# Optimization experiments

Measured on AMD Instinct MI355X. Metric: run time of the kernel, lower is better.

## Reference

```python
import jax, jax.numpy as jnp
import numpy as np

B, L, H, V = 16, 1024, 512, 32000
HALF = H // 2
ALPHA = 0.95
EPS_NORM = 1e-12
EPS_LN = 1e-5


def setup_inputs() -> dict:
    key = jax.random.key(0)
    ks = jax.random.split(key, 12)
    s = 0.02
    return {
        "seq": jax.random.randint(ks[0], (B, L), 0, V),
        "embed": jax.random.normal(ks[1], (V, H), jnp.float32) * s,
        "ff_w1": jax.random.normal(ks[2], (2 * H, H), jnp.float32) * s,
        "ff_b1": jnp.zeros((2 * H,), jnp.float32),
        "ff_w2": jax.random.normal(ks[3], (H, 2 * H), jnp.float32) * s,
        "ff_b2": jnp.zeros((H,), jnp.float32),
        "gamma": jnp.ones((H,), jnp.float32),
        "beta": jnp.zeros((H,), jnp.float32),
        "sem_w": jax.random.normal(ks[4], (HALF, H), jnp.float32) * s,
        "epi_w": jax.random.normal(ks[5], (HALF, H), jnp.float32) * s,
        "rp_w": jax.random.normal(ks[6], (H, H), jnp.float32) * s,
        "rp_b": jnp.zeros((H,), jnp.float32),
        "out_w": jax.random.normal(ks[7], (V, H), jnp.float32) * s,
        "out_b": jnp.zeros((V,), jnp.float32),
    }


def _layernorm(x, gamma, beta):
    mu = jnp.mean(x, axis=-1, keepdims=True)
    var = jnp.mean(jnp.square(x - mu), axis=-1, keepdims=True)
    return (x - mu) * jax.lax.rsqrt(var + EPS_LN) * gamma + beta


def _l2norm(k):
    # F.normalize: k / max(||k||_2, eps)
    n = jnp.sqrt(jnp.sum(jnp.square(k), axis=-1, keepdims=True))
    return k / jnp.maximum(n, EPS_NORM)


def reference(seq, embed, ff_w1, ff_b1, ff_w2, ff_b2, gamma, beta,
              sem_w, epi_w, rp_w, rp_b, out_w, out_b):
    h = embed[seq]  # [B, L, H]
    ff = jnp.maximum(jnp.einsum('blh,fh->blf', h, ff_w1) + ff_b1, 0.0)
    ff = jnp.einsum('blf,hf->blh', ff, ff_w2) + ff_b2
    h = _layernorm(h + ff, gamma, beta)  # [B, L, H]

    # precompute all keys, time-major for scan: [L, B, half]
    ks_all = jnp.einsum('blh,ch->lbc', h, sem_w)
    ke_all = jnp.einsum('blh,ch->lbc', h, epi_w)

    def step(carry, inp):
        Ms, Me = carry                      # [B, half, half]
        ks, ke = inp                        # [B, half]
        kns = _l2norm(ks)
        kne = _l2norm(ke)
        vps = jnp.einsum('bij,bj->bi', Ms, kns)
        vpe = jnp.einsum('bij,bj->bi', Me, kne)
        Ds = (ks - vps)[:, :, None] * kns[:, None, :]
        De = (ke - vpe)[:, :, None] * kne[:, None, :]
        Ms = Ms + (1.0 - ALPHA) * Ds
        Me = Me + (1.0 - ALPHA) * De
        return (Ms, Me), None

    M0 = jnp.zeros((B, HALF, HALF), h.dtype)
    (M_s, M_e), _ = jax.lax.scan(step, (M0, M0), (ks_all[:L - 1], ke_all[:L - 1]))

    qs = ks_all[L - 1]  # sem_p(h[:, -1])
    qe = ke_all[L - 1]  # epi_p(h[:, -1])
    cs = jnp.einsum('bij,bj->bi', M_s, qs)
    ce = jnp.einsum('bij,bj->bi', M_e, qe)
    c = jnp.concatenate([cs, ce], axis=-1)  # [B, H]
    r = jnp.einsum('bh,gh->bg', c, rp_w) + rp_b
    return jnp.einsum('bh,vh->bv', r, out_w) + out_b  # [B, V]
```

## Files before the change

### kernel.cpp

```cpp
#include <hip/hip_runtime.h>
#include <stdint.h>

#define Bsz 16
#define Lsz 1024
#define Hsz 512
#define Vsz 32000
#define HALF 256
#define BETA 0.05f

typedef unsigned short u16;
typedef __attribute__((ext_vector_type(8))) short short8;
typedef __attribute__((ext_vector_type(4))) float f32x4;

__device__ __forceinline__ float bf2f(u16 u) { return __uint_as_float(((unsigned int)u) << 16); }
__device__ __forceinline__ u16 f2bf(float f) {
    unsigned int u = __float_as_uint(f);
    return (u16)((u + 0x7FFFu + ((u >> 16) & 1u)) >> 16);
}
__device__ __forceinline__ bool mode_f32(const void* gamma) {
    return *(const unsigned int*)gamma == 0x3F800000u;
}

__device__ __forceinline__ float wave_sum(float p) {
    p += __shfl_xor(p, 32, 64);
    p += __shfl_xor(p, 16, 64);
    p += __shfl_xor(p, 8, 64);
    p += __shfl_xor(p, 4, 64);
    p += __shfl_xor(p, 2, 64);
    p += __shfl_xor(p, 1, 64);
    return p;
}

__device__ __forceinline__ void cvt8(const void* src, u16* dst, int i, bool f32m) {
    union { u16 u[8]; uint4 q; } o;
    if (f32m) {
        const float* s = (const float*)src + i;
        const float4 a = *(const float4*)s;
        const float4 b = *(const float4*)(s + 4);
        o.u[0] = f2bf(a.x); o.u[1] = f2bf(a.y); o.u[2] = f2bf(a.z); o.u[3] = f2bf(a.w);
        o.u[4] = f2bf(b.x); o.u[5] = f2bf(b.y); o.u[6] = f2bf(b.z); o.u[7] = f2bf(b.w);
    } else {
        o.q = *(const uint4*)((const u16*)src + i);
    }
    *(uint4*)(dst + i) = o.q;
}

__global__ __launch_bounds__(256)
void cvt_all(const void* s0, const void* s1, const void* s2, const void* s3,
             const void* s4, const void* s5, const void* s6, const void* s7,
             const void* s8, const void* s9, const void* s10,
             u16* d0, u16* d1, u16* d2, u16* d3, u16* d4, u16* d5, u16* d6,
             u16* d7, u16* d8, u16* d9, u16* d10, const void* gamma) {
    const bool f32m = mode_f32(gamma);
    const int g = blockIdx.x * 256 + threadIdx.x;
    const void* src; u16* dst; int off;
    if      (g < 65536)  { src = s0;  dst = d0;  off = g; }
    else if (g < 131072) { src = s1;  dst = d1;  off = g - 65536; }
    else if (g < 147456) { src = s2;  dst = d2;  off = g - 131072; }
    else if (g < 163840) { src = s3;  dst = d3;  off = g - 147456; }
    else if (g < 196608) { src = s4;  dst = d4;  off = g - 163840; }
    else if (g < 196736) { src = s5;  dst = d5;  off = g - 196608; }
    else if (g < 196800) { src = s6;  dst = d6;  off = g - 196736; }
    else if (g < 196864) { src = s7;  dst = d7;  off = g - 196800; }
    else if (g < 196928) { src = s8;  dst = d8;  off = g - 196864; }
    else if (g < 196992) { src = s9;  dst = d9;  off = g - 196928; }
    else if (g < 200992) { src = s10; dst = d10; off = g - 196992; }
    else return;
    cvt8(src, dst, off * 8, f32m);
}

__global__ __launch_bounds__(256)
void gather_kernel(const int* __restrict__ seq, const void* __restrict__ embed,
                   u16* __restrict__ h0, const void* __restrict__ gamma) {
    const bool f32m = mode_f32(gamma);
    const int row = blockIdx.x * 4 + (threadIdx.x >> 6);
    const int lane = threadIdx.x & 63;
    const int tok = seq[row];
    union { u16 u[8]; uint4 q; } o;
    if (f32m) {
        const float* e = (const float*)embed + (size_t)tok * Hsz + lane * 8;
        const float4 a = *(const float4*)e;
        const float4 b = *(const float4*)(e + 4);
        o.u[0] = f2bf(a.x); o.u[1] = f2bf(a.y); o.u[2] = f2bf(a.z); o.u[3] = f2bf(a.w);
        o.u[4] = f2bf(b.x); o.u[5] = f2bf(b.y); o.u[6] = f2bf(b.z); o.u[7] = f2bf(b.w);
    } else {
        o.q = *((const uint4*)((const u16*)embed + (size_t)tok * Hsz) + lane);
    }
    *((uint4*)(h0 + (size_t)row * Hsz) + lane) = o.q;
}

template <int EPI>
__global__ __launch_bounds__(256)
void gemm128(const u16* __restrict__ A, const u16* __restrict__ B0,
             const u16* __restrict__ B1, const u16* __restrict__ bias,
             const u16* resid, void* Cout, int M, int N, int K) {
    __shared__ u16 Als[128 * 32];
    __shared__ u16 Bls[128 * 32];
    const int tid = threadIdx.x;
    const int wave = tid >> 6, lane = tid & 63;
    const int m0 = blockIdx.y * 128, n0 = blockIdx.x * 128;

    const u16* Bt;
    if (EPI == 2) Bt = (n0 < HALF) ? (B0 + (size_t)n0 * K) : (B1 + (size_t)(n0 - HALF) * K);
    else          Bt = B0 + (size_t)n0 * K;
    const u16* At = A + (size_t)m0 * K;

    const int wm = wave >> 1, wn = wave & 1;
    const int srow = lane >> 2;
    const int sk = (lane & 3) * 8;
    const int fr = lane & 15;
    const int fq = (lane >> 4) * 8;

    f32x4 acc[4][4];
#pragma unroll
    for (int i = 0; i < 4; i++)
#pragma unroll
        for (int j = 0; j < 4; j++) acc[i][j] = (f32x4){0.f, 0.f, 0.f, 0.f};

    for (int k0 = 0; k0 < K; k0 += 32) {
        __syncthreads();
#pragma unroll
        for (int c = 0; c < 2; c++) {
            const int ch = wave * 2 + c;
            const int row = ch * 16 + srow;
            __builtin_amdgcn_global_load_lds(
                (const __attribute__((address_space(1))) uint32_t*)(At + (size_t)row * K + k0 + sk),
                (__attribute__((address_space(3))) uint32_t*)(&Als[ch * 512]), 16, 0, 0);
            __builtin_amdgcn_global_load_lds(
                (const __attribute__((address_space(1))) uint32_t*)(Bt + (size_t)row * K + k0 + sk),
                (__attribute__((address_space(3))) uint32_t*)(&Bls[ch * 512]), 16, 0, 0);
        }
        __syncthreads();
        short8 af[4], bfr[4];
#pragma unroll
        for (int i = 0; i < 4; i++)
            af[i] = *(const short8*)&Als[(wm * 64 + i * 16 + fr) * 32 + fq];
#pragma unroll
        for (int j = 0; j < 4; j++)
            bfr[j] = *(const short8*)&Bls[(wn * 64 + j * 16 + fr) * 32 + fq];
#pragma unroll
        for (int i = 0; i < 4; i++)
#pragma unroll
            for (int j = 0; j < 4; j++)
                acc[i][j] = __builtin_amdgcn_mfma_f32_16x16x32_bf16(af[i], bfr[j], acc[i][j], 0, 0, 0);
    }

#pragma unroll
    for (int i = 0; i < 4; i++) {
#pragma unroll
        for (int j = 0; j < 4; j++) {
            const int n = n0 + wn * 64 + j * 16 + fr;
#pragma unroll
            for (int r = 0; r < 4; r++) {
                const int m = m0 + wm * 64 + i * 16 + (lane >> 4) * 4 + r;
                float v = acc[i][j][r];
                if (EPI == 0) {
                    v += bf2f(bias[n]);
                    v = v > 0.f ? v : 0.f;
                    ((u16*)Cout)[(size_t)m * N + n] = f2bf(v);
                } else if (EPI == 1) {
                    v += bf2f(bias[n]) + bf2f(resid[(size_t)m * N + n]);
                    ((u16*)Cout)[(size_t)m * N + n] = f2bf(v);
                } else {
                    const int mem = n >> 8, col = n & 255;
                    const int b = m >> 10, t = m & 1023;
                    ((u16*)Cout)[((size_t)(mem * Bsz + b) * Lsz + t) * HALF + col] = f2bf(v);
                }
            }
        }
    }
}

__global__ __launch_bounds__(256)
void ln_kernel(const u16* hs, const u16* __restrict__ gamma,
               const u16* __restrict__ beta, u16* hn) {
    const int row = blockIdx.x * 4 + (threadIdx.x >> 6);
    const int lane = threadIdx.x & 63;
    const uint4 raw = *(const uint4*)(hs + (size_t)row * Hsz + lane * 8);
    const u16* xr = (const u16*)&raw;
    float v[8];
#pragma unroll
    for (int j = 0; j < 8; j++) v[j] = bf2f(xr[j]);
    float s = 0.f;
#pragma unroll
    for (int j = 0; j < 8; j++) s += v[j];
    s = wave_sum(s);
    const float mu = s * (1.f / 512.f);
    float q = 0.f;
#pragma unroll
    for (int j = 0; j < 8; j++) { v[j] -= mu; q += v[j] * v[j]; }
    q = wave_sum(q);
    const float rstd = rsqrtf(q * (1.f / 512.f) + 1e-5f);
    union { u16 u[8]; uint4 qv; } o;
#pragma unroll
    for (int j = 0; j < 8; j++) {
        const int n = lane * 8 + j;
        o.u[j] = f2bf(v[j] * rstd * bf2f(gamma[n]) + bf2f(beta[n]));
    }
    *(uint4*)(hn + (size_t)row * Hsz + lane * 8) = o.qv;
}

__global__ __launch_bounds__(256)
void normalize_kernel(u16* kb, float* __restrict__ norms) {
    const int row = blockIdx.x * 4 + (threadIdx.x >> 6);
    const int lane = threadIdx.x & 63;
    u16* p = kb + (size_t)row * HALF + lane * 4;
    uint2 raw = *(uint2*)p;
    const u16* kp = (const u16*)&raw;
    float f[4];
#pragma unroll
    for (int j = 0; j < 4; j++) f[j] = bf2f(kp[j]);
    float s = f[0]*f[0] + f[1]*f[1] + f[2]*f[2] + f[3]*f[3];
    s = wave_sum(s);
    const float n = fmaxf(sqrtf(s), 1e-12f);
    const float inv = 1.f / n;
    union { u16 u[4]; uint2 q; } o;
#pragma unroll
    for (int j = 0; j < 4; j++) o.u[j] = f2bf(f[j] * inv);
    *(uint2*)p = o.q;
    if (lane == 0) norms[row] = n;
}

__global__ __launch_bounds__(256)
void gram_kernel(const u16* __restrict__ kn, float* __restrict__ G) {
    __shared__ u16 ls[64 * 264];
    const int mb = blockIdx.x, c = blockIdx.y;
    const int tid = threadIdx.x;
    const u16* src = kn + ((size_t)mb * Lsz + c * 64) * HALF;
    {
        const int row = tid >> 2, p = tid & 3;
        const u16* sp = src + row * 256 + p * 64;
        u16* dp = ls + row * 264 + p * 64;
#pragma unroll
        for (int i = 0; i < 8; i++)
            *(uint4*)(dp + i * 8) = *(const uint4*)(sp + i * 8);
    }
    __syncthreads();
    const int wave = tid >> 6, lane = tid & 63;
    const int fr = lane & 15, fq = (lane >> 4) * 8;
    f32x4 acc[4];
#pragma unroll
    for (int j = 0; j < 4; j++) acc[j] = (f32x4){0.f, 0.f, 0.f, 0.f};
    for (int k0 = 0; k0 < 256; k0 += 32) {
        const short8 a = *(const short8*)&ls[(wave * 16 + fr) * 264 + k0 + fq];
#pragma unroll
        for (int j = 0; j < 4; j++) {
            const short8 b = *(const short8*)&ls[(j * 16 + fr) * 264 + k0 + fq];
            acc[j] = __builtin_amdgcn_mfma_f32_16x16x32_bf16(a, b, acc[j], 0, 0, 0);
        }
    }
    float* gout = G + ((size_t)mb * 16 + c) * 4096;
#pragma unroll
    for (int j = 0; j < 4; j++)
#pragma unroll
        for (int r = 0; r < 4; r++)
            gout[(wave * 16 + (lane >> 4) * 4 + r) * 64 + j * 16 + fr] = acc[j][r];
}

__global__ __launch_bounds__(256)
void scan2_kernel(const u16* __restrict__ kn, const float* __restrict__ norms,
                  const float* __restrict__ G, float* __restrict__ cbuf) {
    __shared__ float uL[256], dL[64], sL[64], s2L[64];
    const int mb = blockIdx.x;
    const int tid = threadIdx.x, wave = tid >> 6, lane = tid & 63;
    const u16* knb = kn + (size_t)mb * Lsz * HALF;
    const float* nb = norms + (size_t)mb * Lsz;

    float u = bf2f(knb[1023 * HALF + tid]) * nb[1023];
    float cacc = 0.f;
    uL[tid] = u;
    __syncthreads();

    for (int c = 15; c >= 0; --c) {
        {
            const int t = tid >> 2, p = tid & 3;
            const u16* krow = knb + (size_t)(c * 64 + t) * HALF + p * 64;
            float part = 0.f;
#pragma unroll
            for (int jj = 0; jj < 64; jj += 8) {
                const short8 kv = *(const short8*)(krow + jj);
                const u16* kp = (const u16*)&kv;
                const f32x4 u0 = *(const f32x4*)&uL[p * 64 + jj];
                const f32x4 u1 = *(const f32x4*)&uL[p * 64 + jj + 4];
                part += bf2f(kp[0]) * u0[0] + bf2f(kp[1]) * u0[1]
                      + bf2f(kp[2]) * u0[2] + bf2f(kp[3]) * u0[3]
                      + bf2f(kp[4]) * u1[0] + bf2f(kp[5]) * u1[1]
                      + bf2f(kp[6]) * u1[2] + bf2f(kp[7]) * u1[3];
            }
            part += __shfl_xor(part, 1, 64);
            part += __shfl_xor(part, 2, 64);
            if (p == 0) dL[t] = part;
        }
        __syncthreads();
        if (wave == 0) {
            const float* grow = G + ((size_t)mb * 16 + c) * 4096 + lane * 64;
            float g[64];
#pragma unroll
            for (int q = 0; q < 64; q += 4) {
                const f32x4 gv = *(const f32x4*)(grow + q);
                g[q] = gv[0]; g[q + 1] = gv[1]; g[q + 2] = gv[2]; g[q + 3] = gv[3];
            }
#pragma unroll
            for (int q = 0; q < 64; q++) g[q] = (q > lane) ? g[q] : 0.f;
            const float d = dL[lane];
            const float mynorm = nb[c * 64 + lane];
            float r = 0.f;
            const bool lastchunk = (c == 15);
#pragma unroll
            for (int tp = 63; tp >= 0; --tp) {
                float cand = d - BETA * r;
                if (lastchunk && tp == 63) cand = 0.f;
                const float s = __shfl(cand, tp, 64);
                if (lane == tp) { sL[tp] = s; s2L[tp] = s * mynorm; }
                r += g[tp] * s;
            }
        }
        __syncthreads();
        {
            const u16* kcol = knb + (size_t)c * 64 * HALF + tid;
            float du = 0.f, dc = 0.f;
#pragma unroll 8
            for (int t2 = 0; t2 < 64; t2++) {
                const float kv = bf2f(kcol[(size_t)t2 * HALF]);
                du += sL[t2] * kv;
                dc += s2L[t2] * kv;
            }
            u -= BETA * du;
            cacc += BETA * dc;
            uL[tid] = u;
        }
        __syncthreads();
    }
    const int b = mb & 15, mem = mb >> 4;
    cbuf[(size_t)b * Hsz + mem * HALF + tid] = cacc;
}

__global__ __launch_bounds__(256)
void rproj_kernel(const float* __restrict__ cbuf, const u16* __restrict__ rpw,
                  const u16* __restrict__ rpb, u16* __restrict__ rbuf) {
    __shared__ float cl[Hsz];
    const int b = blockIdx.x, tid = threadIdx.x;
    cl[tid] = cbuf[(size_t)b * Hsz + tid];
    cl[tid + 256] = cbuf[(size_t)b * Hsz + 256 + tid];
    __syncthreads();
#pragma unroll
    for (int gg = 0; gg < 2; gg++) {
        const int g = gg * 256 + tid;
        const u16* wr = rpw + (size_t)g * Hsz;
        float acc = bf2f(rpb[g]);
        for (int k = 0; k < Hsz; k += 8) {
            const uint4 w8 = *(const uint4*)(wr + k);
            const u16* w = (const u16*)&w8;
            const float4 c0 = *(const float4*)&cl[k];
            const float4 c1 = *(const float4*)&cl[k + 4];
            acc += bf2f(w[0]) * c0.x + bf2f(w[1]) * c0.y + bf2f(w[2]) * c0.z + bf2f(w[3]) * c0.w
                 + bf2f(w[4]) * c1.x + bf2f(w[5]) * c1.y + bf2f(w[6]) * c1.z + bf2f(w[7]) * c1.w;
        }
        rbuf[(size_t)b * Hsz + g] = f2bf(acc);
    }
}

__global__ __launch_bounds__(256)
void logits_kernel(const u16* __restrict__ rbuf, const void* __restrict__ outw,
                   const u16* __restrict__ outb, void* __restrict__ out,
                   const void* __restrict__ gamma) {
    __shared__ u16 rls[16 * Hsz];
    const bool f32m = mode_f32(gamma);
    const int tid = threadIdx.x;
    {
        const uint4* src = (const uint4*)rbuf;
        uint4* dst = (uint4*)rls;
#pragma unroll
        for (int i = 0; i < 4; i++) dst[i * 256 + tid] = src[i * 256 + tid];
    }
    __syncthreads();
    const int wave = tid >> 6, lane = tid & 63;
    const int n0 = blockIdx.x * 256 + wave * 64;
    const int fr = lane & 15, fq = (lane >> 4) * 8;
    f32x4 acc[4];
#pragma unroll
    for (int j = 0; j < 4; j++) acc[j] = (f32x4){0.f, 0.f, 0.f, 0.f};
    if (f32m) {
        for (int k0 = 0; k0 < Hsz; k0 += 32) {
            const short8 af = *(const short8*)&rls[fr * Hsz + k0 + fq];
#pragma unroll
            for (int j = 0; j < 4; j++) {
                const float* wp = (const float*)outw + (size_t)(n0 + j * 16 + fr) * Hsz + k0 + fq;
                const float4 a = *(const float4*)wp;
                const float4 bq = *(const float4*)(wp + 4);
                union { u16 u[8]; short8 v; } bb;
                bb.u[0] = f2bf(a.x); bb.u[1] = f2bf(a.y); bb.u[2] = f2bf(a.z); bb.u[3] = f2bf(a.w);
                bb.u[4] = f2bf(bq.x); bb.u[5] = f2bf(bq.y); bb.u[6] = f2bf(bq.z); bb.u[7] = f2bf(bq.w);
                acc[j] = __builtin_amdgcn_mfma_f32_16x16x32_bf16(af, bb.v, acc[j], 0, 0, 0);
            }
        }
    } else {
        for (int k0 = 0; k0 < Hsz; k0 += 32) {
            const short8 af = *(const short8*)&rls[fr * Hsz + k0 + fq];
#pragma unroll
            for (int j = 0; j < 4; j++) {
                const short8 b8 = *(const short8*)((const u16*)outw + (size_t)(n0 + j * 16 + fr) * Hsz + k0 + fq);
                acc[j] = __builtin_amdgcn_mfma_f32_16x16x32_bf16(af, b8, acc[j], 0, 0, 0);
            }
        }
    }
#pragma unroll
    for (int j = 0; j < 4; j++) {
        const int v = n0 + j * 16 + fr;
        const float bv = bf2f(outb[v]);
#pragma unroll
        for (int r = 0; r < 4; r++) {
            const int bb = (lane >> 4) * 4 + r;
            const float val = acc[j][r] + bv;
            if (f32m) ((float*)out)[(size_t)bb * Vsz + v] = val;
            else      ((u16*)out)[(size_t)bb * Vsz + v] = f2bf(val);
        }
    }
}

extern "C" void kernel_launch(void* const* d_in, const int* in_sizes, int n_in,
                              void* d_out, int out_size, void* d_ws, size_t ws_size,
                              hipStream_t stream) {
    const int*  seq   = (const int*)d_in[0];
    const void* embed = d_in[1];
    const void* ffw1  = d_in[2];
    const void* ffb1  = d_in[3];
    const void* ffw2  = d_in[4];
    const void* ffb2  = d_in[5];
    const void* gamma = d_in[6];
    const void* beta  = d_in[7];
    const void* semw  = d_in[8];
    const void* epiw  = d_in[9];
    const void* rpw   = d_in[10];
    const void* rpb   = d_in[11];
    const void* outw  = d_in[12];
    const void* outb  = d_in[13];

    char* ws = (char*)d_ws;
    u16*   h0    = (u16*)(ws + 0);
    u16*   C1    = (u16*)(ws + (size_t)0x1000000);
    u16*   kbuf  = (u16*)(ws + (size_t)0x1000000);
    float* Gbuf  = (float*)(ws + (size_t)0x2000000);
    float* norms = (float*)(ws + (size_t)0x2800000);
    size_t off   = 50331648;
    u16* cffw1 = (u16*)(ws + off); off += (size_t)1024 * 512 * 2;
    u16* cffw2 = (u16*)(ws + off); off += (size_t)512 * 1024 * 2;
    u16* csemw = (u16*)(ws + off); off += (size_t)256 * 512 * 2;
    u16* cepiw = (u16*)(ws + off); off += (size_t)256 * 512 * 2;
    u16* crpw  = (u16*)(ws + off); off += (size_t)512 * 512 * 2;
    u16* cffb1 = (u16*)(ws + off); off += 1024 * 2;
    u16* cffb2 = (u16*)(ws + off); off += 512 * 2;
    u16* cgam  = (u16*)(ws + off); off += 512 * 2;
    u16* cbet  = (u16*)(ws + off); off += 512 * 2;
    u16* crpb  = (u16*)(ws + off); off += 512 * 2;
    u16* coutb = (u16*)(ws + off); off += (size_t)32000 * 2;
    off = (off + 255) & ~(size_t)255;
    float* cbuf = (float*)(ws + off); off += (size_t)16 * 512 * 4;
    u16*   rbuf = (u16*)(ws + off);

    cvt_all<<<786, 256, 0, stream>>>(ffw1, ffw2, semw, epiw, rpw, ffb1, ffb2,
                                     gamma, beta, rpb, outb,
                                     cffw1, cffw2, csemw, cepiw, crpw, cffb1, cffb2,
                                     cgam, cbet, crpb, coutb, gamma);
    gather_kernel<<<4096, 256, 0, stream>>>(seq, embed, h0, gamma);
    gemm128<0><<<dim3(8, 128), 256, 0, stream>>>(h0, cffw1, nullptr, cffb1, nullptr, C1,
                                                 16384, 1024, 512);
    gemm128<1><<<dim3(4, 128), 256, 0, stream>>>(C1, cffw2, nullptr, cffb2, h0, h0,
                                                 16384, 512, 1024);
    ln_kernel<<<4096, 256, 0, stream>>>(h0, cgam, cbet, h0);
    gemm128<2><<<dim3(4, 128), 256, 0, stream>>>(h0, csemw, cepiw, nullptr, nullptr, kbuf,
                                                 16384, 512, 512);
    normalize_kernel<<<8192, 256, 0, stream>>>(kbuf, norms);
    gram_kernel<<<dim3(32, 16), 256, 0, stream>>>(kbuf, Gbuf);
    scan2_kernel<<<32, 256, 0, stream>>>(kbuf, norms, Gbuf, cbuf);
    rproj_kernel<<<16, 256, 0, stream>>>(cbuf, crpw, crpb, rbuf);
    logits_kernel<<<125, 256, 0, stream>>>(rbuf, outw, coutb, d_out, gamma);
}
```

Before: 442.5 us.

## Prefetch next key chunk and G block into LDS with register double-buffering in scan2

The backward scan kernel now stages each 64-row chunk of normalized keys and its Gram block into shared memory. The loads for the next chunk are issued into registers at the start of each iteration and written to LDS after the current chunk finishes. This hides global-memory latency behind the serial per-chunk work and replaces repeated strided global reads with LDS reads. In exchange it uses more LDS and more registers, and adds one extra barrier per chunk.

```diff
diff --git a/kernel.cpp b/kernel.cpp
--- a/kernel.cpp
+++ b/kernel.cpp
@@ -7,6 +7,8 @@
 #define Vsz 32000
 #define HALF 256
 #define BETA 0.05f
+#define LSTRIDE 264
+#define GSTRIDE 68
 
 typedef unsigned short u16;
 typedef __attribute__((ext_vector_type(8))) short short8;
@@ -260,26 +262,54 @@
 __global__ __launch_bounds__(256)
 void scan2_kernel(const u16* __restrict__ kn, const float* __restrict__ norms,
                   const float* __restrict__ G, float* __restrict__ cbuf) {
+    __shared__ u16 ls[64 * LSTRIDE];
+    __shared__ float GS[64 * GSTRIDE];
     __shared__ float uL[256], dL[64], sL[64], s2L[64];
     const int mb = blockIdx.x;
     const int tid = threadIdx.x, wave = tid >> 6, lane = tid & 63;
     const u16* knb = kn + (size_t)mb * Lsz * HALF;
     const float* nb = norms + (size_t)mb * Lsz;
+    const float* gb = G + (size_t)mb * 16 * 4096;
+
+    const int srow = tid >> 2, scol = (tid & 3) * 64;
+    const int gcol = (tid & 3) * 16;
 
     float u = bf2f(knb[1023 * HALF + tid]) * nb[1023];
+    uL[tid] = u;
     float cacc = 0.f;
-    uL[tid] = u;
+
+    {
+        const uint4* s4 = (const uint4*)(knb + (size_t)15 * 64 * HALF + srow * HALF + scol);
+        u16* dp = ls + srow * LSTRIDE + scol;
+#pragma unroll
+        for (int i = 0; i < 8; i++) *(uint4*)(dp + i * 8) = s4[i];
+        const float4* g4 = (const float4*)(gb + (size_t)15 * 4096 + srow * 64 + gcol);
+        float* gp = GS + srow * GSTRIDE + gcol;
+#pragma unroll
+        for (int i = 0; i < 4; i++) *(float4*)(gp + i * 4) = g4[i];
+    }
     __syncthreads();
 
     for (int c = 15; c >= 0; --c) {
+        uint4 kv[8]; float4 gv[4];
+        if (c > 0) {
+            const uint4* s4 = (const uint4*)(knb + (size_t)(c - 1) * 64 * HALF + srow * HALF + scol);
+#pragma unroll
+            for (int i = 0; i < 8; i++) kv[i] = s4[i];
+            const float4* g4 = (const float4*)(gb + (size_t)(c - 1) * 4096 + srow * 64 + gcol);
+#pragma unroll
+            for (int i = 0; i < 4; i++) gv[i] = g4[i];
+        }
+        const float mynorm = (wave == 0) ? nb[c * 64 + lane] : 0.f;
+
         {
             const int t = tid >> 2, p = tid & 3;
-            const u16* krow = knb + (size_t)(c * 64 + t) * HALF + p * 64;
+            const u16* krow = ls + t * LSTRIDE + p * 64;
             float part = 0.f;
 #pragma unroll
             for (int jj = 0; jj < 64; jj += 8) {
-                const short8 kv = *(const short8*)(krow + jj);
-                const u16* kp = (const u16*)&kv;
+                const short8 kvv = *(const short8*)(krow + jj);
+                const u16* kp = (const u16*)&kvv;
                 const f32x4 u0 = *(const f32x4*)&uL[p * 64 + jj];
                 const f32x4 u1 = *(const f32x4*)&uL[p * 64 + jj + 4];
                 part += bf2f(kp[0]) * u0[0] + bf2f(kp[1]) * u0[1]
@@ -293,17 +323,16 @@
         }
         __syncthreads();
         if (wave == 0) {
-            const float* grow = G + ((size_t)mb * 16 + c) * 4096 + lane * 64;
             float g[64];
+            const float* grow = GS + lane * GSTRIDE;
 #pragma unroll
             for (int q = 0; q < 64; q += 4) {
-                const f32x4 gv = *(const f32x4*)(grow + q);
-                g[q] = gv[0]; g[q + 1] = gv[1]; g[q + 2] = gv[2]; g[q + 3] = gv[3];
+                const float4 gq = *(const float4*)(grow + q);
+                g[q] = gq.x; g[q + 1] = gq.y; g[q + 2] = gq.z; g[q + 3] = gq.w;
             }
 #pragma unroll
             for (int q = 0; q < 64; q++) g[q] = (q > lane) ? g[q] : 0.f;
             const float d = dL[lane];
-            const float mynorm = nb[c * 64 + lane];
             float r = 0.f;
             const bool lastchunk = (c == 15);
 #pragma unroll
@@ -317,19 +346,27 @@
         }
         __syncthreads();
         {
-            const u16* kcol = knb + (size_t)c * 64 * HALF + tid;
             float du = 0.f, dc = 0.f;
-#pragma unroll 8
+#pragma unroll
             for (int t2 = 0; t2 < 64; t2++) {
-                const float kv = bf2f(kcol[(size_t)t2 * HALF]);
-                du += sL[t2] * kv;
-                dc += s2L[t2] * kv;
+                const float kv2 = bf2f(ls[t2 * LSTRIDE + tid]);
+                du += sL[t2] * kv2;
+                dc += s2L[t2] * kv2;
             }
             u -= BETA * du;
             cacc += BETA * dc;
             uL[tid] = u;
         }
         __syncthreads();
+        if (c > 0) {
+            u16* dp = ls + srow * LSTRIDE + scol;
+#pragma unroll
+            for (int i = 0; i < 8; i++) *(uint4*)(dp + i * 8) = kv[i];
+            float* gp = GS + srow * GSTRIDE + gcol;
+#pragma unroll
+            for (int i = 0; i < 4; i++) *(float4*)(gp + i * 4) = gv[i];
+            __syncthreads();
+        }
     }
     const int b = mb & 15, mem = mb >> 4;
     cbuf[(size_t)b * Hsz + mem * HALF + tid] = cacc;
```

Result: slower. 476.4 us (+7.7%).
